# Kernel tuning notes

Measured on AMD Instinct MI355X. Metric: run time of the kernel, lower is better.

Reference implementation:

```python
import jax, jax.numpy as jnp
import numpy as np

B, S, D = 4, 2048, 1024
EPS = 1e-5

def setup_inputs() -> dict:
    key = jax.random.key(0)
    ks = jax.random.split(key, 6)
    return {
        "x": jax.random.normal(ks[0], (B, S, D), dtype=jnp.float32),
        "ln_w": jax.random.uniform(ks[1], (D,), dtype=jnp.float32),
        "wq": jax.random.normal(ks[2], (D, D), dtype=jnp.float32) * (1.0 / np.sqrt(D)),
        "wk": jax.random.normal(ks[3], (D, D), dtype=jnp.float32) * (1.0 / np.sqrt(D)),
        "wv": jax.random.normal(ks[4], (D, D), dtype=jnp.float32) * (1.0 / np.sqrt(D)),
        "wo": jax.random.normal(ks[5], (D, D), dtype=jnp.float32) * (1.0 / np.sqrt(D)),
    }

def reference(x, ln_w, wq, wk, wv, wo):
    # LayerNorm (bias=False): normalize over last dim, scale by ln_w
    mu = jnp.mean(x, axis=-1, keepdims=True)
    var = jnp.mean(jnp.square(x - mu), axis=-1, keepdims=True)
    h = (x - mu) * jax.lax.rsqrt(var + EPS) * ln_w
    # QKV projections (torch Linear: y = h @ W.T)
    q = jnp.einsum("bsd,ed->bse", h, wq)
    k = jnp.einsum("bsd,ed->bse", h, wk)
    v = jnp.einsum("bsd,ed->bse", h, wv)
    # Attention: NOTE source has no 1/sqrt(d) scaling
    scores = jnp.einsum("bqd,bkd->bqk", q, k)
    attn = jax.nn.softmax(scores, axis=-1)
    ctx = jnp.einsum("bqk,bkd->bqd", attn, v)
    return jnp.einsum("bsd,ed->bse", ctx, wo)
```

## Files before the change

### kernel.cpp

```cpp
#include <hip/hip_runtime.h>
#include <hip/hip_bf16.h>

using bf16 = __hip_bfloat16;
typedef __attribute__((ext_vector_type(8))) short short8;
typedef __attribute__((ext_vector_type(4))) float f32x4;
typedef __attribute__((ext_vector_type(4))) unsigned short us4;

static constexpr int Bn = 4, Sn = 2048, Dn = 1024;
static constexpr int ROWS = Bn * Sn;
static constexpr float EPS = 1e-5f;

__device__ __forceinline__ void splitf(float v, bf16& hi, bf16& lo) {
    hi = __float2bfloat16(v);
    lo = __float2bfloat16(v - __bfloat162float(hi));
}

__device__ __forceinline__ void gload_lds16(const void* g, void* l) {
    __builtin_amdgcn_global_load_lds(
        (__attribute__((address_space(1))) void*)(void*)g,
        (__attribute__((address_space(3))) void*)l, 16, 0, 0);
}

template <bool LO>
__global__ __launch_bounds__(256) void wsplit_kernel(const float* __restrict__ w,
                                                     bf16* __restrict__ hi,
                                                     bf16* __restrict__ lo, int n4) {
    int i = blockIdx.x * 256 + threadIdx.x;
    if (i >= n4) return;
    float4 v = reinterpret_cast<const float4*>(w)[i];
    int o = i * 4;
    bf16 h, l;
    splitf(v.x, h, l); hi[o+0] = h; if constexpr (LO) lo[o+0] = l;
    splitf(v.y, h, l); hi[o+1] = h; if constexpr (LO) lo[o+1] = l;
    splitf(v.z, h, l); hi[o+2] = h; if constexpr (LO) lo[o+2] = l;
    splitf(v.w, h, l); hi[o+3] = h; if constexpr (LO) lo[o+3] = l;
}

__global__ __launch_bounds__(256) void ln_kernel(const float* __restrict__ x,
                                                 const float* __restrict__ w,
                                                 bf16* __restrict__ hhi,
                                                 bf16* __restrict__ hlo) {
    const int row = blockIdx.x, tid = threadIdx.x;
    const int lane = tid & 63, wave = tid >> 6;
    const float4 v = reinterpret_cast<const float4*>(x + (size_t)row * Dn)[tid];
    float s  = v.x + v.y + v.z + v.w;
    float s2 = v.x*v.x + v.y*v.y + v.z*v.z + v.w*v.w;
    #pragma unroll
    for (int off = 32; off > 0; off >>= 1) {
        s  += __shfl_down(s,  off, 64);
        s2 += __shfl_down(s2, off, 64);
    }
    __shared__ float red[8];
    if (lane == 0) { red[wave] = s; red[4 + wave] = s2; }
    __syncthreads();
    s  = red[0] + red[1] + red[2] + red[3];
    s2 = red[4] + red[5] + red[6] + red[7];
    const float mu  = s * (1.0f / Dn);
    const float var = s2 * (1.0f / Dn) - mu * mu;
    const float rs  = rsqrtf(var + EPS);
    const float4 wv = reinterpret_cast<const float4*>(w)[tid];
    const size_t o = (size_t)row * Dn + tid * 4;
    bf16 h, l;
    splitf((v.x - mu) * rs * wv.x, h, l); hhi[o+0] = h; hlo[o+0] = l;
    splitf((v.y - mu) * rs * wv.y, h, l); hhi[o+1] = h; hlo[o+1] = l;
    splitf((v.z - mu) * rs * wv.z, h, l); hhi[o+2] = h; hlo[o+2] = l;
    splitf((v.w - mu) * rs * wv.w, h, l); hhi[o+3] = h; hlo[o+3] = l;
}

__global__ __launch_bounds__(256) void softmax_kernel(float* __restrict__ scores) {
    const int row = blockIdx.x, tid = threadIdx.x;
    const int lane = tid & 63, wave = tid >> 6;
    float* r = scores + (size_t)row * Sn;
    const float4 v0 = reinterpret_cast<const float4*>(r)[tid];
    const float4 v1 = reinterpret_cast<const float4*>(r)[tid + 256];
    float m = fmaxf(fmaxf(fmaxf(v0.x, v0.y), fmaxf(v0.z, v0.w)),
                    fmaxf(fmaxf(v1.x, v1.y), fmaxf(v1.z, v1.w)));
    #pragma unroll
    for (int off = 32; off > 0; off >>= 1) m = fmaxf(m, __shfl_down(m, off, 64));
    __shared__ float red[8];
    if (lane == 0) red[wave] = m;
    __syncthreads();
    m = fmaxf(fmaxf(red[0], red[1]), fmaxf(red[2], red[3]));
    float e[8];
    e[0] = expf(v0.x - m); e[1] = expf(v0.y - m);
    e[2] = expf(v0.z - m); e[3] = expf(v0.w - m);
    e[4] = expf(v1.x - m); e[5] = expf(v1.y - m);
    e[6] = expf(v1.z - m); e[7] = expf(v1.w - m);
    float s = e[0]+e[1]+e[2]+e[3]+e[4]+e[5]+e[6]+e[7];
    #pragma unroll
    for (int off = 32; off > 0; off >>= 1) s += __shfl_down(s, off, 64);
    if (lane == 0) red[4 + wave] = s;
    __syncthreads();
    s = red[4] + red[5] + red[6] + red[7];
    const float inv = 1.0f / s;
    bf16* hi = reinterpret_cast<bf16*>(r);
    #pragma unroll
    for (int j = 0; j < 4; ++j) hi[tid*4 + j]        = __float2bfloat16(e[j] * inv);
    #pragma unroll
    for (int j = 0; j < 4; ++j) hi[1024 + tid*4 + j] = __float2bfloat16(e[4+j] * inv);
}

template <int NT, int SM>
__global__ __launch_bounds__(256)
void gemm3(const bf16* __restrict__ Ahi, const bf16* __restrict__ Alo, int lda, long long sA,
           const bf16* __restrict__ Bhi, const bf16* __restrict__ Blo, int ldb, long long sB,
           float* __restrict__ Cf, bf16* __restrict__ Chi, bf16* __restrict__ Clo,
           int ldc, long long sC, int K) {
    const int tid = threadIdx.x;
    const int lane = tid & 63, wave = tid >> 6;
    const int bm = blockIdx.x, bn = blockIdx.y;
    const long long aBase = (long long)blockIdx.z * sA;
    const long long bBase = (long long)blockIdx.z * sB;
    const long long cBase = (long long)blockIdx.z * sC;

    __shared__ bf16 sAh[128*32];
    __shared__ bf16 sBh[128*32];
    __shared__ bf16 sAl[NT == 3 ? 128*32 : 64];
    __shared__ bf16 sBl[NT == 3 ? 128*32 : 64];

    f32x4 acc[4][4];
    #pragma unroll
    for (int i = 0; i < 4; ++i)
        #pragma unroll
        for (int j = 0; j < 4; ++j) acc[i][j] = f32x4{0.f, 0.f, 0.f, 0.f};

    const int wm = wave >> 1, wn = wave & 1;
    const int fr = lane & 15;
    const int kb = (lane >> 4) * 8;

    for (int k0 = 0; k0 < K; k0 += 32) {
        #pragma unroll
        for (int i = 0; i < 2; ++i) {
            const int idx = (i * 4 + wave) * 64 + lane;
            const int row = idx >> 2;
            const int seg = (idx & 3) * 8;
            const int lds_off = (i * 4 + wave) * 512;
            const long long ga = aBase + (long long)(bm * 128 + row) * lda + k0 + seg;
            const long long gb = bBase + (long long)(bn * 128 + row) * ldb + k0 + seg;
            gload_lds16(Ahi + ga, sAh + lds_off);
            gload_lds16(Bhi + gb, sBh + lds_off);
            if constexpr (NT == 3) {
                gload_lds16(Alo + ga, sAl + lds_off);
                gload_lds16(Blo + gb, sBl + lds_off);
            }
        }
        __syncthreads();

        short8 ah[4], bh[4];
        #pragma unroll
        for (int t = 0; t < 4; ++t) {
            ah[t] = *reinterpret_cast<const short8*>(sAh + (wm*64 + t*16 + fr) * 32 + kb);
            bh[t] = *reinterpret_cast<const short8*>(sBh + (wn*64 + t*16 + fr) * 32 + kb);
        }
        if constexpr (NT == 3) {
            short8 al[4], bl[4];
            #pragma unroll
            for (int t = 0; t < 4; ++t) {
                al[t] = *reinterpret_cast<const short8*>(sAl + (wm*64 + t*16 + fr) * 32 + kb);
                bl[t] = *reinterpret_cast<const short8*>(sBl + (wn*64 + t*16 + fr) * 32 + kb);
            }
            #pragma unroll
            for (int mi = 0; mi < 4; ++mi)
                #pragma unroll
                for (int ni = 0; ni < 4; ++ni) {
                    acc[mi][ni] = __builtin_amdgcn_mfma_f32_16x16x32_bf16(ah[mi], bh[ni], acc[mi][ni], 0, 0, 0);
                    acc[mi][ni] = __builtin_amdgcn_mfma_f32_16x16x32_bf16(ah[mi], bl[ni], acc[mi][ni], 0, 0, 0);
                    acc[mi][ni] = __builtin_amdgcn_mfma_f32_16x16x32_bf16(al[mi], bh[ni], acc[mi][ni], 0, 0, 0);
                }
        } else {
            #pragma unroll
            for (int mi = 0; mi < 4; ++mi)
                #pragma unroll
                for (int ni = 0; ni < 4; ++ni)
                    acc[mi][ni] = __builtin_amdgcn_mfma_f32_16x16x32_bf16(ah[mi], bh[ni], acc[mi][ni], 0, 0, 0);
        }
        __syncthreads();
    }

    #pragma unroll
    for (int mi = 0; mi < 4; ++mi) {
        const int row0 = bm * 128 + wm * 64 + mi * 16 + (lane >> 4) * 4;
        #pragma unroll
        for (int ni = 0; ni < 4; ++ni) {
            const int col = bn * 128 + wn * 64 + ni * 16 + fr;
            if constexpr (SM == 0) {
                #pragma unroll
                for (int r = 0; r < 4; ++r)
                    Cf[cBase + (long long)(row0 + r) * ldc + col] = acc[mi][ni][r];
            } else if constexpr (SM == 1) {
                #pragma unroll
                for (int r = 0; r < 4; ++r) {
                    bf16 h, l; splitf(acc[mi][ni][r], h, l);
                    const long long o = cBase + (long long)(row0 + r) * ldc + col;
                    Chi[o] = h; Clo[o] = l;
                }
            } else if constexpr (SM == 2) {
                alignas(8) bf16 th[4];
                #pragma unroll
                for (int r = 0; r < 4; ++r) th[r] = __float2bfloat16(acc[mi][ni][r]);
                const long long o = cBase + (long long)col * ldc + row0;
                *reinterpret_cast<us4*>(Chi + o) = *reinterpret_cast<const us4*>(th);
            } else {
                #pragma unroll
                for (int r = 0; r < 4; ++r)
                    Chi[cBase + (long long)(row0 + r) * ldc + col] = __float2bfloat16(acc[mi][ni][r]);
            }
        }
    }
}

extern "C" void kernel_launch(void* const* d_in, const int* in_sizes, int n_in,
                              void* d_out, int out_size, void* d_ws, size_t ws_size,
                              hipStream_t stream) {
    const float* x    = (const float*)d_in[0];
    const float* ln_w = (const float*)d_in[1];
    const float* wq   = (const float*)d_in[2];
    const float* wk   = (const float*)d_in[3];
    const float* wv   = (const float*)d_in[4];
    const float* wo   = (const float*)d_in[5];
    float* out = (float*)d_out;

    const size_t M1 = 1u << 20;
    bf16* base = (bf16*)d_ws;
    bf16* h_hi   = base;
    bf16* h_lo   = base + 8*M1;
    bf16* wqk_hi = base + 16*M1;
    bf16* wqk_lo = base + 18*M1;
    bf16* wv_hi  = base + 20*M1;
    bf16* qk_hi  = base + 32*M1;
    bf16* qk_lo  = base + 48*M1;
    bf16* vt     = base + 64*M1;
    bf16* ctx    = base + 72*M1;
    bf16* wo_hi  = base + 80*M1;
    float* scores = (float*)base;

    const int n4 = (int)(M1 / 4);
    wsplit_kernel<true ><<<dim3(n4/256), 256, 0, stream>>>(wq, wqk_hi,      wqk_lo,      n4);
    wsplit_kernel<true ><<<dim3(n4/256), 256, 0, stream>>>(wk, wqk_hi + M1, wqk_lo + M1, n4);
    wsplit_kernel<false><<<dim3(n4/256), 256, 0, stream>>>(wv, wv_hi, nullptr, n4);
    wsplit_kernel<false><<<dim3(n4/256), 256, 0, stream>>>(wo, wo_hi, nullptr, n4);

    ln_kernel<<<ROWS, 256, 0, stream>>>(x, ln_w, h_hi, h_lo);

    gemm3<3,1><<<dim3(ROWS/128, 2*Dn/128), 256, 0, stream>>>(
        h_hi, h_lo, Dn, 0, wqk_hi, wqk_lo, Dn, 0,
        nullptr, qk_hi, qk_lo, 2*Dn, 0, Dn);

    gemm3<1,2><<<dim3(Sn/128, Dn/128, Bn), 256, 0, stream>>>(
        h_hi, nullptr, Dn, (long long)Sn * Dn, wv_hi, nullptr, Dn, 0,
        nullptr, vt, nullptr, Sn, (long long)Dn * Sn, Dn);

    gemm3<3,0><<<dim3(Sn/128, Sn/128, Bn), 256, 0, stream>>>(
        qk_hi, qk_lo, 2*Dn, (long long)Sn * 2*Dn,
        qk_hi + Dn, qk_lo + Dn, 2*Dn, (long long)Sn * 2*Dn,
        scores, nullptr, nullptr, Sn, (long long)Sn * Sn, Dn);

    softmax_kernel<<<ROWS, 256, 0, stream>>>(scores);

    gemm3<1,3><<<dim3(Sn/128, Dn/128, Bn), 256, 0, stream>>>(
        (const bf16*)scores, nullptr, 2*Sn, (long long)Sn * 2*Sn,
        vt, nullptr, Sn, (long long)Dn * Sn,
        nullptr, ctx, nullptr, Dn, (long long)Sn * Dn, Sn);

    gemm3<1,0><<<dim3(ROWS/128, Dn/128), 256, 0, stream>>>(
        ctx, nullptr, Dn, 0, wo_hi, nullptr, Dn, 0,
        out, nullptr, nullptr, Dn, 0, Dn);
}
```

Measured before the change: 473.7 us.

## Fold split-bf16 terms into K dimension and add 256x256 pipelined GEMM

Instead of issuing three MFMAs per tile on separate hi/lo buffers, the hi and lo parts are concatenated along K (a 3072-wide LN output and a 3072-wide weight layout), so the three-term product becomes one plain bf16 GEMM. A new 512-thread, 256x256-tile GEMM uses triple-buffered LDS with swizzling, split barriers and setprio to overlap loads with MFMAs. It is used for the QK projection and for the scores GEMM, which runs as two passes with the second accumulating into the fp32 output. This trades extra K length and an extra read-modify-write pass over the scores for larger tiles and better load/compute overlap. The workspace is also reorganized to reuse buffers.

```diff
diff --git a/kernel.cpp b/kernel.cpp
--- a/kernel.cpp
+++ b/kernel.cpp
@@ -21,25 +21,34 @@
         (__attribute__((address_space(3))) void*)l, 16, 0, 0);
 }
 
-template <bool LO>
-__global__ __launch_bounds__(256) void wsplit_kernel(const float* __restrict__ w,
-                                                     bf16* __restrict__ hi,
-                                                     bf16* __restrict__ lo, int n4) {
-    int i = blockIdx.x * 256 + threadIdx.x;
-    if (i >= n4) return;
-    float4 v = reinterpret_cast<const float4*>(w)[i];
-    int o = i * 4;
-    bf16 h, l;
-    splitf(v.x, h, l); hi[o+0] = h; if constexpr (LO) lo[o+0] = l;
-    splitf(v.y, h, l); hi[o+1] = h; if constexpr (LO) lo[o+1] = l;
-    splitf(v.z, h, l); hi[o+2] = h; if constexpr (LO) lo[o+2] = l;
-    splitf(v.w, h, l); hi[o+3] = h; if constexpr (LO) lo[o+3] = l;
-}
-
-__global__ __launch_bounds__(256) void ln_kernel(const float* __restrict__ x,
-                                                 const float* __restrict__ w,
-                                                 bf16* __restrict__ hhi,
-                                                 bf16* __restrict__ hlo) {
+__global__ __launch_bounds__(256) void wsplit3_kernel(const float* __restrict__ w,
+                                                      bf16* __restrict__ out) {
+    const int i = blockIdx.x * 256 + threadIdx.x;
+    const float4 v = reinterpret_cast<const float4*>(w)[i];
+    const int row = i >> 8, c = (i & 255) << 2;
+    alignas(8) bf16 h[4], l[4];
+    splitf(v.x, h[0], l[0]); splitf(v.y, h[1], l[1]);
+    splitf(v.z, h[2], l[2]); splitf(v.w, h[3], l[3]);
+    bf16* o = out + (size_t)row * 3072 + c;
+    *reinterpret_cast<us4*>(o)        = *reinterpret_cast<const us4*>(h);
+    *reinterpret_cast<us4*>(o + 1024) = *reinterpret_cast<const us4*>(h);
+    *reinterpret_cast<us4*>(o + 2048) = *reinterpret_cast<const us4*>(l);
+}
+
+__global__ __launch_bounds__(256) void wsplit_hi_kernel(const float* __restrict__ w,
+                                                        bf16* __restrict__ hi) {
+    const int i = blockIdx.x * 256 + threadIdx.x;
+    const float4 v = reinterpret_cast<const float4*>(w)[i];
+    alignas(8) bf16 h[4];
+    bf16 l;
+    splitf(v.x, h[0], l); splitf(v.y, h[1], l);
+    splitf(v.z, h[2], l); splitf(v.w, h[3], l);
+    *reinterpret_cast<us4*>(hi + i * 4) = *reinterpret_cast<const us4*>(h);
+}
+
+__global__ __launch_bounds__(256) void ln3_kernel(const float* __restrict__ x,
+                                                  const float* __restrict__ w,
+                                                  bf16* __restrict__ h3) {
     const int row = blockIdx.x, tid = threadIdx.x;
     const int lane = tid & 63, wave = tid >> 6;
     const float4 v = reinterpret_cast<const float4*>(x + (size_t)row * Dn)[tid];
@@ -59,12 +68,15 @@
     const float var = s2 * (1.0f / Dn) - mu * mu;
     const float rs  = rsqrtf(var + EPS);
     const float4 wv = reinterpret_cast<const float4*>(w)[tid];
-    const size_t o = (size_t)row * Dn + tid * 4;
-    bf16 h, l;
-    splitf((v.x - mu) * rs * wv.x, h, l); hhi[o+0] = h; hlo[o+0] = l;
-    splitf((v.y - mu) * rs * wv.y, h, l); hhi[o+1] = h; hlo[o+1] = l;
-    splitf((v.z - mu) * rs * wv.z, h, l); hhi[o+2] = h; hlo[o+2] = l;
-    splitf((v.w - mu) * rs * wv.w, h, l); hhi[o+3] = h; hlo[o+3] = l;
+    alignas(8) bf16 h[4], l[4];
+    splitf((v.x - mu) * rs * wv.x, h[0], l[0]);
+    splitf((v.y - mu) * rs * wv.y, h[1], l[1]);
+    splitf((v.z - mu) * rs * wv.z, h[2], l[2]);
+    splitf((v.w - mu) * rs * wv.w, h[3], l[3]);
+    bf16* o = h3 + (size_t)row * 3072 + tid * 4;
+    *reinterpret_cast<us4*>(o)        = *reinterpret_cast<const us4*>(h);
+    *reinterpret_cast<us4*>(o + 1024) = *reinterpret_cast<const us4*>(l);
+    *reinterpret_cast<us4*>(o + 2048) = *reinterpret_cast<const us4*>(h);
 }
 
 __global__ __launch_bounds__(256) void softmax_kernel(float* __restrict__ scores) {
@@ -100,11 +112,11 @@
     for (int j = 0; j < 4; ++j) hi[1024 + tid*4 + j] = __float2bfloat16(e[4+j] * inv);
 }
 
-template <int NT, int SM>
+template <int SM>
 __global__ __launch_bounds__(256)
-void gemm3(const bf16* __restrict__ Ahi, const bf16* __restrict__ Alo, int lda, long long sA,
-           const bf16* __restrict__ Bhi, const bf16* __restrict__ Blo, int ldb, long long sB,
-           float* __restrict__ Cf, bf16* __restrict__ Chi, bf16* __restrict__ Clo,
+void gemm3(const bf16* __restrict__ A, int lda, long long sA,
+           const bf16* __restrict__ B, int ldb, long long sB,
+           float* __restrict__ Cf, bf16* __restrict__ Cb,
            int ldc, long long sC, int K) {
     const int tid = threadIdx.x;
     const int lane = tid & 63, wave = tid >> 6;
@@ -115,8 +127,6 @@
 
     __shared__ bf16 sAh[128*32];
     __shared__ bf16 sBh[128*32];
-    __shared__ bf16 sAl[NT == 3 ? 128*32 : 64];
-    __shared__ bf16 sBl[NT == 3 ? 128*32 : 64];
 
     f32x4 acc[4][4];
     #pragma unroll
@@ -135,45 +145,21 @@
             const int row = idx >> 2;
             const int seg = (idx & 3) * 8;
             const int lds_off = (i * 4 + wave) * 512;
-            const long long ga = aBase + (long long)(bm * 128 + row) * lda + k0 + seg;
-            const long long gb = bBase + (long long)(bn * 128 + row) * ldb + k0 + seg;
-            gload_lds16(Ahi + ga, sAh + lds_off);
-            gload_lds16(Bhi + gb, sBh + lds_off);
-            if constexpr (NT == 3) {
-                gload_lds16(Alo + ga, sAl + lds_off);
-                gload_lds16(Blo + gb, sBl + lds_off);
-            }
+            gload_lds16(A + aBase + (long long)(bm * 128 + row) * lda + k0 + seg, sAh + lds_off);
+            gload_lds16(B + bBase + (long long)(bn * 128 + row) * ldb + k0 + seg, sBh + lds_off);
         }
         __syncthreads();
-
         short8 ah[4], bh[4];
         #pragma unroll
         for (int t = 0; t < 4; ++t) {
             ah[t] = *reinterpret_cast<const short8*>(sAh + (wm*64 + t*16 + fr) * 32 + kb);
             bh[t] = *reinterpret_cast<const short8*>(sBh + (wn*64 + t*16 + fr) * 32 + kb);
         }
-        if constexpr (NT == 3) {
-            short8 al[4], bl[4];
+        #pragma unroll
+        for (int mi = 0; mi < 4; ++mi)
             #pragma unroll
-            for (int t = 0; t < 4; ++t) {
-                al[t] = *reinterpret_cast<const short8*>(sAl + (wm*64 + t*16 + fr) * 32 + kb);
-                bl[t] = *reinterpret_cast<const short8*>(sBl + (wn*64 + t*16 + fr) * 32 + kb);
-            }
-            #pragma unroll
-            for (int mi = 0; mi < 4; ++mi)
-                #pragma unroll
-                for (int ni = 0; ni < 4; ++ni) {
-                    acc[mi][ni] = __builtin_amdgcn_mfma_f32_16x16x32_bf16(ah[mi], bh[ni], acc[mi][ni], 0, 0, 0);
-                    acc[mi][ni] = __builtin_amdgcn_mfma_f32_16x16x32_bf16(ah[mi], bl[ni], acc[mi][ni], 0, 0, 0);
-                    acc[mi][ni] = __builtin_amdgcn_mfma_f32_16x16x32_bf16(al[mi], bh[ni], acc[mi][ni], 0, 0, 0);
-                }
-        } else {
-            #pragma unroll
-            for (int mi = 0; mi < 4; ++mi)
-                #pragma unroll
-                for (int ni = 0; ni < 4; ++ni)
-                    acc[mi][ni] = __builtin_amdgcn_mfma_f32_16x16x32_bf16(ah[mi], bh[ni], acc[mi][ni], 0, 0, 0);
-        }
+            for (int ni = 0; ni < 4; ++ni)
+                acc[mi][ni] = __builtin_amdgcn_mfma_f32_16x16x32_bf16(ah[mi], bh[ni], acc[mi][ni], 0, 0, 0);
         __syncthreads();
     }
 
@@ -187,23 +173,141 @@
                 #pragma unroll
                 for (int r = 0; r < 4; ++r)
                     Cf[cBase + (long long)(row0 + r) * ldc + col] = acc[mi][ni][r];
-            } else if constexpr (SM == 1) {
-                #pragma unroll
-                for (int r = 0; r < 4; ++r) {
-                    bf16 h, l; splitf(acc[mi][ni][r], h, l);
-                    const long long o = cBase + (long long)(row0 + r) * ldc + col;
-                    Chi[o] = h; Clo[o] = l;
-                }
             } else if constexpr (SM == 2) {
                 alignas(8) bf16 th[4];
                 #pragma unroll
                 for (int r = 0; r < 4; ++r) th[r] = __float2bfloat16(acc[mi][ni][r]);
                 const long long o = cBase + (long long)col * ldc + row0;
-                *reinterpret_cast<us4*>(Chi + o) = *reinterpret_cast<const us4*>(th);
+                *reinterpret_cast<us4*>(Cb + o) = *reinterpret_cast<const us4*>(th);
             } else {
                 #pragma unroll
                 for (int r = 0; r < 4; ++r)
-                    Chi[cBase + (long long)(row0 + r) * ldc + col] = __float2bfloat16(acc[mi][ni][r]);
+                    Cb[cBase + (long long)(row0 + r) * ldc + col] = __float2bfloat16(acc[mi][ni][r]);
+            }
+        }
+    }
+}
+
+template <int SM>
+__global__ __launch_bounds__(512, 2)
+void gemm8(const bf16* __restrict__ A, int lda, long long sA,
+           const bf16* __restrict__ B, int ldb, long long sB,
+           float* __restrict__ Cf, bf16* __restrict__ Cq, bf16* __restrict__ Ck,
+           int ldc, long long sC, int K) {
+    const int tid = threadIdx.x;
+    const int lane = tid & 63, wave = tid >> 6;
+    const int wm = wave >> 2, wn = wave & 3;
+    const int fl = lane & 15, s0 = lane >> 4;
+    const int bm = blockIdx.x, bn = blockIdx.y;
+
+    __shared__ bf16 lds[3 * 16384];
+
+    const int tr = tid >> 2;
+    const int sg = (tid & 3) ^ ((tr >> 1) & 3);
+    const bf16* gA = A + (long long)blockIdx.z * sA + (long long)(bm*256 + tr) * lda + sg*8;
+    const bf16* gB = B + (long long)blockIdx.z * sB + (long long)(bn*256 + tr) * ldb + sg*8;
+    bf16* ldsw = lds + wave * 512;
+    const long long a128 = (long long)128 * lda, b128 = (long long)128 * ldb;
+
+    const int sw = (s0 ^ ((fl >> 1) & 3)) * 8;
+    const int aoff = (wm*128 + fl) * 32 + sw;
+    const int boff = 8192 + (wn*64 + fl) * 32 + sw;
+
+    f32x4 acc[8][4];
+    #pragma unroll
+    for (int i = 0; i < 8; ++i)
+        #pragma unroll
+        for (int j = 0; j < 4; ++j) acc[i][j] = f32x4{0.f, 0.f, 0.f, 0.f};
+
+    const int NT = K >> 5;
+    gload_lds16(gA,             ldsw);
+    gload_lds16(gA + a128,      ldsw + 4096);
+    gload_lds16(gB,             ldsw + 8192);
+    gload_lds16(gB + b128,      ldsw + 12288);
+    gload_lds16(gA + 32,        ldsw + 16384);
+    gload_lds16(gA + a128 + 32, ldsw + 16384 + 4096);
+    gload_lds16(gB + 32,        ldsw + 16384 + 8192);
+    gload_lds16(gB + b128 + 32, ldsw + 16384 + 12288);
+    asm volatile("s_waitcnt vmcnt(4)" ::: "memory");
+    __builtin_amdgcn_s_barrier();
+
+    int c0 = 0;
+    for (int kt = 0; kt < NT; ++kt) {
+        const int c2 = (c0 >= 1) ? c0 - 1 : 2;
+        int ktp = kt + 2; if (ktp >= NT) ktp = 0;
+        const int kp = ktp << 5;
+        const bf16* ab = lds + c0 * 16384;
+        bf16* pw = ldsw + c2 * 16384;
+
+        gload_lds16(gA + kp,        pw);
+        gload_lds16(gA + kp + a128, pw + 4096);
+        short8 bfr[4], afr[4];
+        #pragma unroll
+        for (int ni = 0; ni < 4; ++ni) bfr[ni] = *reinterpret_cast<const short8*>(ab + boff + ni*512);
+        #pragma unroll
+        for (int mi = 0; mi < 4; ++mi) afr[mi] = *reinterpret_cast<const short8*>(ab + aoff + mi*512);
+        __builtin_amdgcn_s_barrier();
+        __builtin_amdgcn_s_setprio(1);
+        #pragma unroll
+        for (int mi = 0; mi < 4; ++mi)
+            #pragma unroll
+            for (int ni = 0; ni < 4; ++ni)
+                acc[mi][ni] = __builtin_amdgcn_mfma_f32_16x16x32_bf16(afr[mi], bfr[ni], acc[mi][ni], 0, 0, 0);
+        __builtin_amdgcn_s_setprio(0);
+        __builtin_amdgcn_s_barrier();
+
+        gload_lds16(gB + kp,        pw + 8192);
+        gload_lds16(gB + kp + b128, pw + 12288);
+        short8 af2[4];
+        #pragma unroll
+        for (int mi = 0; mi < 4; ++mi) af2[mi] = *reinterpret_cast<const short8*>(ab + aoff + (mi+4)*512);
+        __builtin_amdgcn_s_barrier();
+        __builtin_amdgcn_s_setprio(1);
+        #pragma unroll
+        for (int mi = 0; mi < 4; ++mi)
+            #pragma unroll
+            for (int ni = 0; ni < 4; ++ni)
+                acc[mi+4][ni] = __builtin_amdgcn_mfma_f32_16x16x32_bf16(af2[mi], bfr[ni], acc[mi+4][ni], 0, 0, 0);
+        __builtin_amdgcn_s_setprio(0);
+        asm volatile("s_waitcnt vmcnt(4)" ::: "memory");
+        __builtin_amdgcn_s_barrier();
+        c0 = (c0 < 2) ? c0 + 1 : 0;
+    }
+
+    const long long cB = (long long)blockIdx.z * sC;
+    #pragma unroll
+    for (int mi = 0; mi < 8; ++mi) {
+        const int row0 = bm*256 + wm*128 + mi*16 + s0*4;
+        #pragma unroll
+        for (int ni = 0; ni < 4; ++ni) {
+            const int col = bn*256 + wn*64 + ni*16 + fl;
+            if constexpr (SM == 0) {
+                #pragma unroll
+                for (int r = 0; r < 4; ++r)
+                    Cf[cB + (long long)(row0 + r) * ldc + col] = acc[mi][ni][r];
+            } else if constexpr (SM == 4) {
+                #pragma unroll
+                for (int r = 0; r < 4; ++r) {
+                    const long long o = cB + (long long)(row0 + r) * ldc + col;
+                    Cf[o] += acc[mi][ni][r];
+                }
+            } else {
+                if (col < 1024) {
+                    #pragma unroll
+                    for (int r = 0; r < 4; ++r) {
+                        bf16 h, l; splitf(acc[mi][ni][r], h, l);
+                        const long long o = (long long)(row0 + r) * ldc + col;
+                        Cq[o] = l; Cq[o + 1024] = h;
+                    }
+                } else {
+                    const int c = col - 1024;
+                    #pragma unroll
+                    for (int r = 0; r < 4; ++r) {
+                        bf16 h, l; splitf(acc[mi][ni][r], h, l);
+                        const long long o = (long long)(row0 + r) * ldc + c;
+                        Ck[o] = h; Ck[o + 1024] = l;
+                    }
+                }
             }
         }
     }
@@ -222,47 +326,47 @@
 
     const size_t M1 = 1u << 20;
     bf16* base = (bf16*)d_ws;
-    bf16* h_hi   = base;
-    bf16* h_lo   = base + 8*M1;
-    bf16* wqk_hi = base + 16*M1;
-    bf16* wqk_lo = base + 18*M1;
-    bf16* wv_hi  = base + 20*M1;
-    bf16* qk_hi  = base + 32*M1;
-    bf16* qk_lo  = base + 48*M1;
-    bf16* vt     = base + 64*M1;
-    bf16* ctx    = base + 72*M1;
-    bf16* wo_hi  = base + 80*M1;
+    bf16* h3    = base;
+    bf16* wqk3  = base + 24*M1;
+    bf16* wv_hi = base + 30*M1;
     float* scores = (float*)base;
-
-    const int n4 = (int)(M1 / 4);
-    wsplit_kernel<true ><<<dim3(n4/256), 256, 0, stream>>>(wq, wqk_hi,      wqk_lo,      n4);
-    wsplit_kernel<true ><<<dim3(n4/256), 256, 0, stream>>>(wk, wqk_hi + M1, wqk_lo + M1, n4);
-    wsplit_kernel<false><<<dim3(n4/256), 256, 0, stream>>>(wv, wv_hi, nullptr, n4);
-    wsplit_kernel<false><<<dim3(n4/256), 256, 0, stream>>>(wo, wo_hi, nullptr, n4);
-
-    ln_kernel<<<ROWS, 256, 0, stream>>>(x, ln_w, h_hi, h_lo);
-
-    gemm3<3,1><<<dim3(ROWS/128, 2*Dn/128), 256, 0, stream>>>(
-        h_hi, h_lo, Dn, 0, wqk_hi, wqk_lo, Dn, 0,
-        nullptr, qk_hi, qk_lo, 2*Dn, 0, Dn);
-
-    gemm3<1,2><<<dim3(Sn/128, Dn/128, Bn), 256, 0, stream>>>(
-        h_hi, nullptr, Dn, (long long)Sn * Dn, wv_hi, nullptr, Dn, 0,
-        nullptr, vt, nullptr, Sn, (long long)Dn * Sn, Dn);
-
-    gemm3<3,0><<<dim3(Sn/128, Sn/128, Bn), 256, 0, stream>>>(
-        qk_hi, qk_lo, 2*Dn, (long long)Sn * 2*Dn,
-        qk_hi + Dn, qk_lo + Dn, 2*Dn, (long long)Sn * 2*Dn,
-        scores, nullptr, nullptr, Sn, (long long)Sn * Sn, Dn);
+    bf16* q2    = base + 32*M1;
+    bf16* k2    = base + 48*M1;
+    bf16* vt    = base + 64*M1;
+    bf16* ctx   = base + 32*M1;
+    bf16* wo_hi = base + 40*M1;
+
+    wsplit3_kernel<<<dim3(1024), 256, 0, stream>>>(wq, wqk3);
+    wsplit3_kernel<<<dim3(1024), 256, 0, stream>>>(wk, wqk3 + (size_t)1024 * 3072);
+    wsplit_hi_kernel<<<dim3(1024), 256, 0, stream>>>(wv, wv_hi);
+
+    ln3_kernel<<<ROWS, 256, 0, stream>>>(x, ln_w, h3);
+
+    gemm8<1><<<dim3(ROWS/256, 2*Dn/256), 512, 0, stream>>>(
+        h3, 3072, 0, wqk3, 3072, 0,
+        nullptr, q2, k2, 2048, 0, 3072);
+
+    gemm3<2><<<dim3(Sn/128, Dn/128, Bn), 256, 0, stream>>>(
+        h3, 3072, (long long)Sn * 3072, wv_hi, 1024, 0,
+        nullptr, vt, Sn, (long long)Dn * Sn, 1024);
+
+    gemm8<0><<<dim3(Sn/256, Sn/256, Bn), 512, 0, stream>>>(
+        q2, 2048, (long long)Sn * 2048, k2, 2048, (long long)Sn * 2048,
+        scores, nullptr, nullptr, Sn, (long long)Sn * Sn, 2048);
+    gemm8<4><<<dim3(Sn/256, Sn/256, Bn), 512, 0, stream>>>(
+        q2 + 1024, 2048, (long long)Sn * 2048, k2, 2048, (long long)Sn * 2048,
+        scores, nullptr, nullptr, Sn, (long long)Sn * Sn, 1024);
 
     softmax_kernel<<<ROWS, 256, 0, stream>>>(scores);
 
-    gemm3<1,3><<<dim3(Sn/128, Dn/128, Bn), 256, 0, stream>>>(
-        (const bf16*)scores, nullptr, 2*Sn, (long long)Sn * 2*Sn,
-        vt, nullptr, Sn, (long long)Dn * Sn,
-        nullptr, ctx, nullptr, Dn, (long long)Sn * Dn, Sn);
-
-    gemm3<1,0><<<dim3(ROWS/128, Dn/128), 256, 0, stream>>>(
-        ctx, nullptr, Dn, 0, wo_hi, nullptr, Dn, 0,
-        out, nullptr, nullptr, Dn, 0, Dn);
-}
+    wsplit_hi_kernel<<<dim3(1024), 256, 0, stream>>>(wo, wo_hi);
+
+    gemm3<3><<<dim3(Sn/128, Dn/128, Bn), 256, 0, stream>>>(
+        (const bf16*)scores, 2*Sn, (long long)Sn * 2*Sn,
+        vt, Sn, (long long)Dn * Sn,
+        nullptr, ctx, Dn, (long long)Sn * Dn, Sn);
+
+    gemm3<0><<<dim3(ROWS/128, Dn/128), 256, 0, stream>>>(
+        ctx, Dn, 0, wo_hi, Dn, 0,
+        out, nullptr, Dn, 0, Dn);
+}
```

Measured after the change: 465.7 us. Within noise of the previous version (-1.7%).
